# Kernel tuning notes

Hardware: AMD Instinct MI355X
Metric: run time of the kernel (lower is better)

Reference implementation:

```python
import jax, jax.numpy as jnp
import numpy as np

NUM_SLOTS = 8
SLOT_DIM = 64
HIDDEN_DIM = 128  # max(slot_dim, 128)
ITERS = 3
EPS = 1e-08
LN_EPS = 1e-05


def _ln(x, w, b):
    mu = jnp.mean(x, axis=-1, keepdims=True)
    var = jnp.mean(jnp.square(x - mu), axis=-1, keepdims=True)
    return (x - mu) * jax.lax.rsqrt(var + LN_EPS) * w + b


def setup_inputs() -> dict:
    key = jax.random.key(0)
    ks = jax.random.split(key, 16)
    b, n, d, h, n_s = 64, 4096, SLOT_DIM, HIDDEN_DIM, NUM_SLOTS
    s = 1.0 / np.sqrt(d)
    sh = 1.0 / np.sqrt(h)
    inp = {
        'inputs': jax.random.normal(ks[0], (b, n, d), jnp.float32),
        'mask': jax.random.randint(ks[1], (b, n), 0, 2, jnp.int32),
        'noise': jax.random.normal(ks[2], (b, n_s, d), jnp.float32),
        'slots_mu': jax.random.normal(ks[3], (1, 1, d), jnp.float32),
        'slots_sigma': jax.random.uniform(ks[4], (1, 1, d), jnp.float32),
        'Wq': jax.random.normal(ks[5], (d, d), jnp.float32) * s,
        'bq': jnp.zeros((d,), jnp.float32),
        'Wk': jax.random.normal(ks[6], (d, d), jnp.float32) * s,
        'bk': jnp.zeros((d,), jnp.float32),
        'Wv': jax.random.normal(ks[7], (d, d), jnp.float32) * s,
        'bv': jnp.zeros((d,), jnp.float32),
        'W_ih': jax.random.normal(ks[8], (3 * d, d), jnp.float32) * s,
        'b_ih': jnp.zeros((3 * d,), jnp.float32),
        'W_hh': jax.random.normal(ks[9], (3 * d, d), jnp.float32) * s,
        'b_hh': jnp.zeros((3 * d,), jnp.float32),
        'W1': jax.random.normal(ks[10], (h, d), jnp.float32) * s,
        'b1': jnp.zeros((h,), jnp.float32),
        'W2': jax.random.normal(ks[11], (d, h), jnp.float32) * sh,
        'b2': jnp.zeros((d,), jnp.float32),
        'ln_in_w': jnp.ones((d,), jnp.float32), 'ln_in_b': jnp.zeros((d,), jnp.float32),
        'ln_s_w': jnp.ones((d,), jnp.float32), 'ln_s_b': jnp.zeros((d,), jnp.float32),
        'ln_ff_w': jnp.ones((d,), jnp.float32), 'ln_ff_b': jnp.zeros((d,), jnp.float32),
    }
    return inp


def reference(inputs, mask, noise, slots_mu, slots_sigma, Wq, bq, Wk, bk, Wv, bv,
              W_ih, b_ih, W_hh, b_hh, W1, b1, W2, b2,
              ln_in_w, ln_in_b, ln_s_w, ln_s_b, ln_ff_w, ln_ff_b):
    b, n, d = inputs.shape
    scale = d ** (-0.5)
    # slots ~ Normal(mu, sigma) via reparameterization with fixed noise
    slots = slots_mu + slots_sigma * noise  # [b, n_s, d]
    m = (mask[:, :, None] != 0)  # [b, n, 1]
    x = _ln(inputs, ln_in_w, ln_in_b)
    k = x @ Wk.T + bk  # [b, n, d]
    v = x @ Wv.T + bv  # [b, n, d]
    for _ in range(ITERS):
        slots_prev = slots
        s_n = _ln(slots, ln_s_w, ln_s_b)
        q = s_n @ Wq.T + bq  # [b, n_s, d]
        dots = jnp.einsum('bid,bjd->bij', k, q) * scale  # [b, n, n_s]
        attn = jax.nn.softmax(dots, axis=-1) + EPS
        attn = jnp.where(m, attn, 0.0)
        attn = attn / jnp.sum(attn, axis=-2, keepdims=True)
        updates = jnp.einsum('bij,bid->bjd', attn, v)  # [b, n_s, d]
        # GRUCell(updates, slots_prev)
        gx = updates @ W_ih.T + b_ih  # [b, n_s, 3d]
        gh = slots_prev @ W_hh.T + b_hh
        xr, xz, xn = jnp.split(gx, 3, axis=-1)
        hr, hz, hn = jnp.split(gh, 3, axis=-1)
        r = jax.nn.sigmoid(xr + hr)
        z = jax.nn.sigmoid(xz + hz)
        nn_ = jnp.tanh(xn + r * hn)
        slots = (1.0 - z) * nn_ + z * slots_prev
        # residual MLP
        ff = _ln(slots, ln_ff_w, ln_ff_b)
        slots = slots + (jax.nn.relu(ff @ W1.T + b1) @ W2.T + b2)
    return slots
```

## Files before the change

kernel.cpp:

```cpp
#include <hip/hip_runtime.h>
#include <hip/hip_bf16.h>

typedef unsigned short u16;
typedef unsigned int u32;
typedef unsigned long long u64;

#define BB 64
#define NN 4096
#define DD 64
#define NSLOT 8
#define HH 128
#define NITER 3

#define BF16_ONES_PROBE 0x3F803F80u

#define OFF_BQ   53248
#define OFF_BK   53312
#define OFF_BV   53376
#define OFF_BIH  53440
#define OFF_BHH  53632
#define OFF_B1   53824
#define OFF_B2   53952
#define OFF_LIW  54016
#define OFF_LIB  54080
#define OFF_LSW  54144
#define OFF_LSB  54208
#define OFF_LFW  54272
#define OFF_LFB  54336
#define OFF_PK   58496

__device__ __forceinline__ float bf2f(u16 u) {
    union { u32 i; float f; } c; c.i = ((u32)u) << 16; return c.f;
}
__device__ __forceinline__ float bflo(u32 w) {
    union { u32 i; float f; } c; c.i = w << 16; return c.f;
}
__device__ __forceinline__ float bfhi(u32 w) {
    union { u32 i; float f; } c; c.i = w & 0xffff0000u; return c.f;
}
__device__ __forceinline__ u16 f2bf(float f) {
    __hip_bfloat16 h = __float2bfloat16(f);
    return *reinterpret_cast<u16*>(&h);
}
__device__ __forceinline__ float ldf(const void* p, int i, bool isbf) {
    return isbf ? bf2f(((const u16*)p)[i]) : ((const float*)p)[i];
}

__device__ __forceinline__ float wsum64(float x) {
    #pragma unroll
    for (int o = 32; o > 0; o >>= 1) x += __shfl_xor(x, o);
    return x;
}

__device__ __forceinline__ float ln64(float v, const float* __restrict__ g,
                                      const float* __restrict__ b, int lane) {
    float mu = wsum64(v) * (1.f / 64.f);
    float d = v - mu;
    float var = wsum64(d * d) * (1.f / 64.f);
    return d * rsqrtf(var + 1e-5f) * g[lane] + b[lane];
}

__device__ __forceinline__ float mat64q(const float* __restrict__ xs,
                                        const float* __restrict__ P,
                                        int lane, int wq) {
    const float4* p4 = (const float4*)P;
    const float4* x4 = (const float4*)xs;
    int c0 = wq << 2;
    float4 x0 = x4[c0], x1 = x4[c0 + 1], x2 = x4[c0 + 2], x3 = x4[c0 + 3];
    float4 w0 = p4[c0 * 64 + lane];
    float4 w1 = p4[(c0 + 1) * 64 + lane];
    float4 w2 = p4[(c0 + 2) * 64 + lane];
    float4 w3 = p4[(c0 + 3) * 64 + lane];
    float a0 = w0.x * x0.x + w0.y * x0.y + w0.z * x0.z + w0.w * x0.w;
    float a1 = w1.x * x1.x + w1.y * x1.y + w1.z * x1.z + w1.w * x1.w;
    float a2 = w2.x * x2.x + w2.y * x2.y + w2.z * x2.z + w2.w * x2.w;
    float a3 = w3.x * x3.x + w3.y * x3.y + w3.z * x3.z + w3.w * x3.w;
    return (a0 + a1) + (a2 + a3);
}

struct PrepArgs {
    const void* w[7];
    const void* v[13];
};

__global__ __launch_bounds__(256) void prep_w(PrepArgs a, float* __restrict__ wf,
                                              const u32* __restrict__ probe) {
    bool isbf = (*probe == BF16_ONES_PROBE);
    int idx = blockIdx.x * 256 + threadIdx.x;
    if (idx < 13 * 4096) {
        int blk = idx >> 12, r = idx & 4095;
        int c = r >> 8, rem = r & 255, j = rem >> 2, dd = rem & 3;
        int m = 4 * c + dd;
        float val;
        if      (blk == 0)  val = ldf(a.w[2], j * 64 + m, isbf);
        else if (blk == 1)  val = ldf(a.w[0], j * 64 + m, isbf);
        else if (blk == 2)  val = ldf(a.w[1], m * 64 + j, isbf);
        else if (blk < 6)   val = ldf(a.w[3], ((blk - 3) * 64 + j) * 64 + m, isbf);
        else if (blk < 9)   val = ldf(a.w[4], ((blk - 6) * 64 + j) * 64 + m, isbf);
        else if (blk < 11)  val = ldf(a.w[5], ((blk - 9) * 64 + j) * 64 + m, isbf);
        else                val = ldf(a.w[6], j * 128 + (blk - 11) * 64 + m, isbf);
        wf[OFF_PK + idx] = val;
    } else {
        int k = idx - 13 * 4096;
        const int voff[13] = {OFF_BQ, OFF_BK, OFF_BV, OFF_BIH, OFF_BHH, OFF_B1, OFF_B2,
                              OFF_LIW, OFF_LIB, OFF_LSW, OFF_LSB, OFF_LFW, OFF_LFB};
        const int vn[13]   = {64, 64, 64, 192, 192, 128, 64, 64, 64, 64, 64, 64, 64};
        #pragma unroll
        for (int t = 0; t < 13; t++) {
            if (k < vn[t]) { wf[voff[t] + k] = ldf(a.v[t], k, isbf); return; }
            k -= vn[t];
        }
    }
}

__device__ __forceinline__ void emit_qstate4(
        float qv, int b, int s, int bs, int lane, int wave,
        const float* __restrict__ wf, float* __restrict__ xa,
        float (*__restrict__ red)[64],
        float* __restrict__ gqp, float* __restrict__ Avec, float* __restrict__ Cvec) {
    if (wave == 0) xa[lane] = qv;
    __syncthreads();
    red[wave][lane] = mat64q(xa, wf + OFF_PK + 2 * 4096, lane, wave);
    __syncthreads();
    float qkv = red[0][lane] + red[1][lane] + red[2][lane] + red[3][lane];
    float gqv = wf[OFF_LIW + lane] * qkv;
    if (wave == 0) gqp[(b << 9) + (lane >> 2) * 32 + s * 4 + (lane & 3)] = gqv;
    float A  = wsum64(gqv);
    float bd = wsum64(qv * wf[OFF_BK + lane]);
    float cq = wsum64(wf[OFF_LIB + lane] * qkv);
    if (wave == 0 && lane == 0) { Avec[bs] = A; Cvec[bs] = cq + bd; }
}

__global__ __launch_bounds__(256, 1) void init_slots(
        const void* __restrict__ noise, const void* __restrict__ mu, const void* __restrict__ sg,
        const float* __restrict__ wf, float* __restrict__ slots,
        float* __restrict__ gqp, float* __restrict__ Avec, float* __restrict__ Cvec,
        float* __restrict__ acc1, float* __restrict__ ssv, float* __restrict__ A2v,
        const u32* __restrict__ probe) {
    __shared__ __align__(16) float xa[64];
    __shared__ float red[4][64];
    bool isbf = (*probe == BF16_ONES_PROBE);
    int bs = blockIdx.x;
    int b = bs >> 3, s = bs & 7;
    int tid = threadIdx.x, wave = tid >> 6, lane = tid & 63;
    int idx = bs * DD + lane;
    float sl = ldf(mu, lane, isbf) + ldf(sg, lane, isbf) * ldf(noise, idx, isbf);
    if (wave == 0) {
        slots[idx] = sl;
        acc1[idx] = 0.f;
        if (lane == 0) { ssv[bs] = 0.f; A2v[bs] = 0.f; }
    }
    float sn = ln64(sl, wf + OFF_LSW, wf + OFF_LSB, lane);
    if (wave == 0) xa[lane] = sn;
    __syncthreads();
    red[wave][lane] = mat64q(xa, wf + OFF_PK + 1 * 4096, lane, wave);
    __syncthreads();
    float qv = wf[OFF_BQ + lane] + red[0][lane] + red[1][lane] + red[2][lane] + red[3][lane];
    emit_qstate4(qv, b, s, bs, lane, wave, wf, xa, red, gqp, Avec, Cvec);
}

__global__ __launch_bounds__(256) void fused_attn(
        const void* __restrict__ xin, const int* __restrict__ mask,
        const float* __restrict__ gqp, const float* __restrict__ Avec,
        const float* __restrict__ Cvec,
        float* __restrict__ acc1, float* __restrict__ ssv, float* __restrict__ A2v,
        const u32* __restrict__ probe) {
    __shared__ float4 gq_s[128];
    __shared__ float4 aw4[256][2];
    __shared__ float racc[4][NSLOT][64];
    __shared__ float rss[4][NSLOT];
    __shared__ float rA2[4][NSLOT];
    __shared__ u64 wmask[4];

    bool isbf = (*probe == BF16_ONES_PROBE);
    int b = blockIdx.x >> 4;
    int base = (blockIdx.x & 15) << 8;
    int tid = threadIdx.x;
    int wave = tid >> 6, lane = tid & 63;

    if (tid < 128) gq_s[tid] = ((const float4*)(gqp + ((size_t)b << 9)))[tid];

    size_t gt = ((size_t)b << 12) + base + tid;
    int mk = mask[gt];
    uint4 xrg[8];
    if (mk && isbf) {
        const uint4* xr = (const uint4*)((const u16*)xin + gt * 64);
        #pragma unroll
        for (int i = 0; i < 8; i++) xrg[i] = xr[i];
    }
    __syncthreads();

    float sum = 0.f, sq = 0.f;
    float d[8] = {0.f, 0.f, 0.f, 0.f, 0.f, 0.f, 0.f, 0.f};
    if (mk) {
        if (isbf) {
            #pragma unroll
            for (int c = 0; c < 16; c++) {
                u32 wa = (c & 1) ? xrg[c >> 1].z : xrg[c >> 1].x;
                u32 wb = (c & 1) ? xrg[c >> 1].w : xrg[c >> 1].y;
                float x0 = bflo(wa), x1 = bfhi(wa), x2 = bflo(wb), x3 = bfhi(wb);
                sum += x0 + x1 + x2 + x3;
                sq  += x0 * x0 + x1 * x1 + x2 * x2 + x3 * x3;
                #pragma unroll
                for (int s = 0; s < 8; s++) {
                    float4 q = gq_s[c * 8 + s];
                    d[s] += q.x * x0 + q.y * x1 + q.z * x2 + q.w * x3;
                }
            }
        } else {
            const float4* xr = (const float4*)((const float*)xin + gt * 64);
            #pragma unroll
            for (int c = 0; c < 16; c++) {
                float4 xv = xr[c];
                sum += xv.x + xv.y + xv.z + xv.w;
                sq  += xv.x * xv.x + xv.y * xv.y + xv.z * xv.z + xv.w * xv.w;
                #pragma unroll
                for (int s = 0; s < 8; s++) {
                    float4 q = gq_s[c * 8 + s];
                    d[s] += q.x * xv.x + q.y * xv.y + q.z * xv.z + q.w * xv.w;
                }
            }
        }
    }
    float muv = sum * (1.f / 64.f);
    float var = sq * (1.f / 64.f) - muv * muv;
    float rs = rsqrtf(var + 1e-5f);
    const float* Av = Avec + (b << 3);
    const float* Cv = Cvec + (b << 3);
    #pragma unroll
    for (int s = 0; s < 8; s++)
        d[s] = 0.125f * (rs * d[s] - rs * muv * Av[s] + Cv[s]);

    float mx = d[0];
    #pragma unroll
    for (int s = 1; s < 8; s++) mx = fmaxf(mx, d[s]);
    float den = 0.f;
    #pragma unroll
    for (int s = 0; s < 8; s++) { d[s] = expf(d[s] - mx); den += d[s]; }
    float inv = 1.f / den;
    float attn[8], aw[8];
    #pragma unroll
    for (int s = 0; s < 8; s++) {
        attn[s] = (mk != 0) ? (d[s] * inv + 1e-8f) : 0.f;
        aw[s] = attn[s] * rs;
    }
    {
        float4 w0; w0.x = aw[0]; w0.y = aw[1]; w0.z = aw[2]; w0.w = aw[3];
        float4 w1; w1.x = aw[4]; w1.y = aw[5]; w1.z = aw[6]; w1.w = aw[7];
        aw4[tid][0] = w0;
        aw4[tid][1] = w1;
    }
    u64 bal = __ballot(mk != 0);
    if (lane == 0) wmask[wave] = bal;
    #pragma unroll
    for (int s = 0; s < 8; s++) {
        float t1 = wsum64(attn[s]);
        float t2 = wsum64(aw[s] * muv);
        if (lane == 0) { rss[wave][s] = t1; rA2[wave][s] = t2; }
    }
    __syncthreads();

    u64 bits = wmask[wave];
    float acc[8] = {0.f, 0.f, 0.f, 0.f, 0.f, 0.f, 0.f, 0.f};
    size_t rowbase = ((size_t)b << 12) + base + (wave << 6);
    const u16* xb16 = (const u16*)xin + rowbase * 64 + lane;
    const float* xf32 = (const float*)xin + rowbase * 64 + lane;
    #pragma unroll 8
    for (int t = 0; t < 64; t++) {
        if ((bits >> t) & 1ULL) {
            float xv = isbf ? bf2f(xb16[t * 64]) : xf32[t * 64];
            float4 a0 = aw4[(wave << 6) + t][0];
            float4 a1 = aw4[(wave << 6) + t][1];
            acc[0] += a0.x * xv; acc[1] += a0.y * xv;
            acc[2] += a0.z * xv; acc[3] += a0.w * xv;
            acc[4] += a1.x * xv; acc[5] += a1.y * xv;
            acc[6] += a1.z * xv; acc[7] += a1.w * xv;
        }
    }
    #pragma unroll
    for (int s = 0; s < 8; s++) racc[wave][s][lane] = acc[s];
    __syncthreads();
    if (wave == 0) {
        float* ag = acc1 + ((size_t)b << 9);
        #pragma unroll
        for (int s = 0; s < 8; s++) {
            float v = racc[0][s][lane] + racc[1][s][lane] + racc[2][s][lane] + racc[3][s][lane];
            atomicAdd(ag + s * 64 + lane, v);
        }
        if (lane < NSLOT) {
            float t1 = rss[0][lane] + rss[1][lane] + rss[2][lane] + rss[3][lane];
            float t2 = rA2[0][lane] + rA2[1][lane] + rA2[2][lane] + rA2[3][lane];
            atomicAdd(ssv + (b << 3) + lane, t1);
            atomicAdd(A2v + (b << 3) + lane, t2);
        }
    }
}

__global__ __launch_bounds__(256, 1) void finalize_k(
        const float* __restrict__ wf, float* __restrict__ acc1, float* __restrict__ ssv,
        float* __restrict__ A2v, float* __restrict__ slots,
        float* __restrict__ gqp, float* __restrict__ Avec, float* __restrict__ Cvec,
        void* __restrict__ out, int last, const u32* __restrict__ probe) {
    __shared__ __align__(16) float xa[64];
    __shared__ __align__(16) float xb[64];
    __shared__ float red[6][4][64];
    bool isbf = (*probe == BF16_ONES_PROBE);
    int bs = blockIdx.x;
    int b = bs >> 3, s = bs & 7;
    int tid = threadIdx.x, wave = tid >> 6, lane = tid & 63;
    int idx = bs * DD + lane;
    const float* P = wf + OFF_PK;

    float sm   = ssv[bs];
    float a2v_ = A2v[bs];
    float ac   = acc1[idx];
    float sp   = slots[idx];

    float un = wf[OFF_LIW + lane] * (ac - a2v_) / sm + wf[OFF_LIB + lane];
    if (wave == 0) xa[lane] = un;
    __syncthreads();
    if (wave == 0) {
        acc1[idx] = 0.f;
        if (lane == 0) { ssv[bs] = 0.f; A2v[bs] = 0.f; }
    }

    red[0][wave][lane] = mat64q(xa, P + 0 * 4096, lane, wave);
    __syncthreads();
    #define SUM4(k) (red[k][0][lane] + red[k][1][lane] + red[k][2][lane] + red[k][3][lane])
    float uv = wf[OFF_BV + lane] + SUM4(0);
    if (wave == 0) { xa[lane] = uv; xb[lane] = sp; }
    __syncthreads();

    red[0][wave][lane] = mat64q(xa, P + 3 * 4096, lane, wave);
    red[1][wave][lane] = mat64q(xa, P + 4 * 4096, lane, wave);
    red[2][wave][lane] = mat64q(xa, P + 5 * 4096, lane, wave);
    red[3][wave][lane] = mat64q(xb, P + 6 * 4096, lane, wave);
    red[4][wave][lane] = mat64q(xb, P + 7 * 4096, lane, wave);
    red[5][wave][lane] = mat64q(xb, P + 8 * 4096, lane, wave);
    __syncthreads();
    float gxr = wf[OFF_BIH + lane]       + SUM4(0);
    float gxz = wf[OFF_BIH + 64 + lane]  + SUM4(1);
    float gxn = wf[OFF_BIH + 128 + lane] + SUM4(2);
    float ghr = wf[OFF_BHH + lane]       + SUM4(3);
    float ghz = wf[OFF_BHH + 64 + lane]  + SUM4(4);
    float ghn = wf[OFF_BHH + 128 + lane] + SUM4(5);
    float r = 1.f / (1.f + expf(-(gxr + ghr)));
    float z = 1.f / (1.f + expf(-(gxz + ghz)));
    float nn = tanhf(gxn + r * ghn);
    float snew = (1.f - z) * nn + z * sp;

    float ff = ln64(snew, wf + OFF_LFW, wf + OFF_LFB, lane);
    if (wave == 0) xa[lane] = ff;
    __syncthreads();
    red[0][wave][lane] = mat64q(xa, P + 9 * 4096, lane, wave);
    red[1][wave][lane] = mat64q(xa, P + 10 * 4096, lane, wave);
    __syncthreads();
    float h1a = fmaxf(wf[OFF_B1 + lane] + SUM4(0), 0.f);
    float h1b = fmaxf(wf[OFF_B1 + 64 + lane] + SUM4(1), 0.f);
    if (wave == 0) { xa[lane] = h1a; xb[lane] = h1b; }
    __syncthreads();
    red[0][wave][lane] = mat64q(xa, P + 11 * 4096, lane, wave)
                       + mat64q(xb, P + 12 * 4096, lane, wave);
    __syncthreads();
    float o = snew + wf[OFF_B2 + lane] + SUM4(0);

    if (wave == 0) slots[idx] = o;
    if (last) {
        if (wave == 0) {
            if (isbf) ((u16*)out)[idx] = f2bf(o);
            else      ((float*)out)[idx] = o;
        }
    } else {
        float sn2 = ln64(o, wf + OFF_LSW, wf + OFF_LSB, lane);
        if (wave == 0) xa[lane] = sn2;
        __syncthreads();
        red[0][wave][lane] = mat64q(xa, P + 1 * 4096, lane, wave);
        __syncthreads();
        float qv = wf[OFF_BQ + lane] + SUM4(0);
        emit_qstate4(qv, b, s, bs, lane, wave, wf, xa, red[0], gqp, Avec, Cvec);
    }
    #undef SUM4
}

extern "C" void kernel_launch(void* const* d_in, const int* in_sizes, int n_in,
                              void* d_out, int out_size, void* d_ws, size_t ws_size,
                              hipStream_t stream) {
    const void* xin   = d_in[0];
    const int* mask   = (const int*)d_in[1];
    const void* noise = d_in[2];
    const void* mu    = d_in[3];
    const void* sg    = d_in[4];
    const u32* probe  = (const u32*)d_in[19];

    char* ws = (char*)d_ws;
    float* wf = (float*)ws;

    size_t o = 524288;
    float* gqp   = (float*)(ws + o); o += (size_t)BB * 512 * 4;
    float* Avec  = (float*)(ws + o); o += (size_t)BB * NSLOT * 4;
    float* Cvec  = (float*)(ws + o); o += (size_t)BB * NSLOT * 4;
    float* acc1  = (float*)(ws + o); o += (size_t)BB * NSLOT * DD * 4;
    float* ssv   = (float*)(ws + o); o += (size_t)BB * NSLOT * 4;
    float* A2v   = (float*)(ws + o); o += (size_t)BB * NSLOT * 4;
    float* slots = (float*)(ws + o); o += (size_t)BB * NSLOT * DD * 4;

    PrepArgs pa;
    pa.w[0] = d_in[5];
    pa.w[1] = d_in[7];
    pa.w[2] = d_in[9];
    pa.w[3] = d_in[11];
    pa.w[4] = d_in[13];
    pa.w[5] = d_in[15];
    pa.w[6] = d_in[17];
    static const int vidx[13] = {6, 8, 10, 12, 14, 16, 18, 19, 20, 21, 22, 23, 24};
    for (int j = 0; j < 13; j++) pa.v[j] = d_in[vidx[j]];

    prep_w<<<213, 256, 0, stream>>>(pa, wf, probe);
    init_slots<<<BB * NSLOT, 256, 0, stream>>>(noise, mu, sg, wf, slots,
                                               gqp, Avec, Cvec, acc1, ssv, A2v, probe);

    for (int it = 0; it < NITER; it++) {
        fused_attn<<<BB * 16, 256, 0, stream>>>(xin, mask, gqp, Avec, Cvec,
                                                acc1, ssv, A2v, probe);
        finalize_k<<<BB * NSLOT, 256, 0, stream>>>(wf, acc1, ssv, A2v, slots,
                                                   gqp, Avec, Cvec,
                                                   d_out, it == NITER - 1 ? 1 : 0, probe);
    }
}
```

Baseline: 260.1 us.

## Fuse slot finalize into attention kernel via last-block-done counter

Removes the separate finalize kernel per iteration. The last of the 16 attention blocks for each batch, detected through an atomic done-counter, now runs the GRU, MLP and next-query update in-kernel. Each wave handles two slots and does the small matvecs with wave shuffles instead of shared memory and block barriers. This saves three kernel launches and the tail waits between them. In exchange the finalize work is serialized into one block per batch, and correctness relies on atomic acquire/release ordering of the accumulator reads.

```diff
diff --git a/kernel.cpp b/kernel.cpp
--- a/kernel.cpp
+++ b/kernel.cpp
@@ -58,6 +58,18 @@
     float d = v - mu;
     float var = wsum64(d * d) * (1.f / 64.f);
     return d * rsqrtf(var + 1e-5f) * g[lane] + b[lane];
+}
+
+__device__ __forceinline__ float mat64p(float xv, const float* __restrict__ P, int lane) {
+    const float4* p4 = (const float4*)P;
+    float acc = 0.f;
+    #pragma unroll
+    for (int c = 0; c < 16; c++) {
+        float4 w = p4[c * 64 + lane];
+        acc += w.x * __shfl(xv, 4 * c + 0) + w.y * __shfl(xv, 4 * c + 1)
+             + w.z * __shfl(xv, 4 * c + 2) + w.w * __shfl(xv, 4 * c + 3);
+    }
+    return acc;
 }
 
 __device__ __forceinline__ float mat64q(const float* __restrict__ xs,
@@ -136,7 +148,7 @@
         const float* __restrict__ wf, float* __restrict__ slots,
         float* __restrict__ gqp, float* __restrict__ Avec, float* __restrict__ Cvec,
         float* __restrict__ acc1, float* __restrict__ ssv, float* __restrict__ A2v,
-        const u32* __restrict__ probe) {
+        u32* __restrict__ done_cnt, const u32* __restrict__ probe) {
     __shared__ __align__(16) float xa[64];
     __shared__ float red[4][64];
     bool isbf = (*probe == BF16_ONES_PROBE);
@@ -149,6 +161,7 @@
         slots[idx] = sl;
         acc1[idx] = 0.f;
         if (lane == 0) { ssv[bs] = 0.f; A2v[bs] = 0.f; }
+        if (s == 0 && lane < NITER) done_cnt[b * NITER + lane] = 0u;
     }
     float sn = ln64(sl, wf + OFF_LSW, wf + OFF_LSB, lane);
     if (wave == 0) xa[lane] = sn;
@@ -159,18 +172,115 @@
     emit_qstate4(qv, b, s, bs, lane, wave, wf, xa, red, gqp, Avec, Cvec);
 }
 
-__global__ __launch_bounds__(256) void fused_attn(
+__device__ void fin_slot(int b, int s, int lane, const float* __restrict__ wf,
+                         float* __restrict__ acc1, float* __restrict__ ssv,
+                         float* __restrict__ A2v, float* __restrict__ slots,
+                         float* __restrict__ gqp, float* __restrict__ Avec,
+                         float* __restrict__ Cvec, void* __restrict__ out,
+                         int last, bool isbf) {
+    int bs = b * NSLOT + s;
+    int idx = bs * DD + lane;
+    const float* P = wf + OFF_PK;
+
+    float sm = 0.f, a2 = 0.f;
+    if (lane == 0) {
+        sm = atomicExch(ssv + bs, 0.f);
+        a2 = atomicExch(A2v + bs, 0.f);
+    }
+    sm = __shfl(sm, 0);
+    a2 = __shfl(a2, 0);
+    float ac = atomicExch(acc1 + idx, 0.f);
+    float sp = slots[idx];
+
+    float un = wf[OFF_LIW + lane] * (ac - a2) / sm + wf[OFF_LIB + lane];
+    float uv = wf[OFF_BV + lane] + mat64p(un, P + 0 * 4096, lane);
+
+    float gxr = wf[OFF_BIH + lane], gxz = wf[OFF_BIH + 64 + lane], gxn = wf[OFF_BIH + 128 + lane];
+    float ghr = wf[OFF_BHH + lane], ghz = wf[OFF_BHH + 64 + lane], ghn = wf[OFF_BHH + 128 + lane];
+    const float4* pxr = (const float4*)(P + 3 * 4096);
+    const float4* pxz = (const float4*)(P + 4 * 4096);
+    const float4* pxn = (const float4*)(P + 5 * 4096);
+    const float4* phr = (const float4*)(P + 6 * 4096);
+    const float4* phz = (const float4*)(P + 7 * 4096);
+    const float4* phn = (const float4*)(P + 8 * 4096);
+    #pragma unroll
+    for (int c = 0; c < 16; c++) {
+        float u0 = __shfl(uv, 4 * c + 0), u1 = __shfl(uv, 4 * c + 1);
+        float u2 = __shfl(uv, 4 * c + 2), u3 = __shfl(uv, 4 * c + 3);
+        float p0 = __shfl(sp, 4 * c + 0), p1 = __shfl(sp, 4 * c + 1);
+        float p2 = __shfl(sp, 4 * c + 2), p3 = __shfl(sp, 4 * c + 3);
+        float4 a;
+        a = pxr[c * 64 + lane]; gxr += a.x * u0 + a.y * u1 + a.z * u2 + a.w * u3;
+        a = pxz[c * 64 + lane]; gxz += a.x * u0 + a.y * u1 + a.z * u2 + a.w * u3;
+        a = pxn[c * 64 + lane]; gxn += a.x * u0 + a.y * u1 + a.z * u2 + a.w * u3;
+        a = phr[c * 64 + lane]; ghr += a.x * p0 + a.y * p1 + a.z * p2 + a.w * p3;
+        a = phz[c * 64 + lane]; ghz += a.x * p0 + a.y * p1 + a.z * p2 + a.w * p3;
+        a = phn[c * 64 + lane]; ghn += a.x * p0 + a.y * p1 + a.z * p2 + a.w * p3;
+    }
+    float r = 1.f / (1.f + expf(-(gxr + ghr)));
+    float z = 1.f / (1.f + expf(-(gxz + ghz)));
+    float nn = tanhf(gxn + r * ghn);
+    float snew = (1.f - z) * nn + z * sp;
+
+    float ff = ln64(snew, wf + OFF_LFW, wf + OFF_LFB, lane);
+    float h1a = wf[OFF_B1 + lane], h1b = wf[OFF_B1 + 64 + lane];
+    const float4* p1a = (const float4*)(P + 9 * 4096);
+    const float4* p1b = (const float4*)(P + 10 * 4096);
+    #pragma unroll
+    for (int c = 0; c < 16; c++) {
+        float f0 = __shfl(ff, 4 * c + 0), f1 = __shfl(ff, 4 * c + 1);
+        float f2 = __shfl(ff, 4 * c + 2), f3 = __shfl(ff, 4 * c + 3);
+        float4 a;
+        a = p1a[c * 64 + lane]; h1a += a.x * f0 + a.y * f1 + a.z * f2 + a.w * f3;
+        a = p1b[c * 64 + lane]; h1b += a.x * f0 + a.y * f1 + a.z * f2 + a.w * f3;
+    }
+    h1a = fmaxf(h1a, 0.f);
+    h1b = fmaxf(h1b, 0.f);
+    float o = snew + wf[OFF_B2 + lane];
+    const float4* p2a = (const float4*)(P + 11 * 4096);
+    const float4* p2b = (const float4*)(P + 12 * 4096);
+    #pragma unroll
+    for (int c = 0; c < 16; c++) {
+        float a0 = __shfl(h1a, 4 * c + 0), a1 = __shfl(h1a, 4 * c + 1);
+        float a2_ = __shfl(h1a, 4 * c + 2), a3 = __shfl(h1a, 4 * c + 3);
+        float b0 = __shfl(h1b, 4 * c + 0), b1 = __shfl(h1b, 4 * c + 1);
+        float b2 = __shfl(h1b, 4 * c + 2), b3 = __shfl(h1b, 4 * c + 3);
+        float4 a;
+        a = p2a[c * 64 + lane]; o += a.x * a0 + a.y * a1 + a.z * a2_ + a.w * a3;
+        a = p2b[c * 64 + lane]; o += a.x * b0 + a.y * b1 + a.z * b2 + a.w * b3;
+    }
+
+    slots[idx] = o;
+    if (last) {
+        if (isbf) ((u16*)out)[idx] = f2bf(o);
+        else      ((float*)out)[idx] = o;
+    } else {
+        float sn2 = ln64(o, wf + OFF_LSW, wf + OFF_LSB, lane);
+        float qv = wf[OFF_BQ + lane] + mat64p(sn2, P + 1 * 4096, lane);
+        float qkv = mat64p(qv, P + 2 * 4096, lane);
+        float gqv = wf[OFF_LIW + lane] * qkv;
+        gqp[(b << 9) + (lane >> 2) * 32 + s * 4 + (lane & 3)] = gqv;
+        float A  = wsum64(gqv);
+        float bd = wsum64(qv * wf[OFF_BK + lane]);
+        float cq = wsum64(wf[OFF_LIB + lane] * qkv);
+        if (lane == 0) { Avec[bs] = A; Cvec[bs] = cq + bd; }
+    }
+}
+
+__global__ __launch_bounds__(256) void attn_fin(
         const void* __restrict__ xin, const int* __restrict__ mask,
-        const float* __restrict__ gqp, const float* __restrict__ Avec,
-        const float* __restrict__ Cvec,
+        const float* __restrict__ wf,
+        float* __restrict__ gqp, float* __restrict__ Avec, float* __restrict__ Cvec,
         float* __restrict__ acc1, float* __restrict__ ssv, float* __restrict__ A2v,
-        const u32* __restrict__ probe) {
+        float* __restrict__ slots, void* __restrict__ out,
+        u32* __restrict__ done_cnt, const u32* __restrict__ probe, int it) {
     __shared__ float4 gq_s[128];
     __shared__ float4 aw4[256][2];
     __shared__ float racc[4][NSLOT][64];
     __shared__ float rss[4][NSLOT];
     __shared__ float rA2[4][NSLOT];
     __shared__ u64 wmask[4];
+    __shared__ int do_fin;
 
     bool isbf = (*probe == BF16_ONES_PROBE);
     int b = blockIdx.x >> 4;
@@ -294,92 +404,20 @@
             atomicAdd(A2v + (b << 3) + lane, t2);
         }
     }
-}
-
-__global__ __launch_bounds__(256, 1) void finalize_k(
-        const float* __restrict__ wf, float* __restrict__ acc1, float* __restrict__ ssv,
-        float* __restrict__ A2v, float* __restrict__ slots,
-        float* __restrict__ gqp, float* __restrict__ Avec, float* __restrict__ Cvec,
-        void* __restrict__ out, int last, const u32* __restrict__ probe) {
-    __shared__ __align__(16) float xa[64];
-    __shared__ __align__(16) float xb[64];
-    __shared__ float red[6][4][64];
-    bool isbf = (*probe == BF16_ONES_PROBE);
-    int bs = blockIdx.x;
-    int b = bs >> 3, s = bs & 7;
-    int tid = threadIdx.x, wave = tid >> 6, lane = tid & 63;
-    int idx = bs * DD + lane;
-    const float* P = wf + OFF_PK;
-
-    float sm   = ssv[bs];
-    float a2v_ = A2v[bs];
-    float ac   = acc1[idx];
-    float sp   = slots[idx];
-
-    float un = wf[OFF_LIW + lane] * (ac - a2v_) / sm + wf[OFF_LIB + lane];
-    if (wave == 0) xa[lane] = un;
-    __syncthreads();
-    if (wave == 0) {
-        acc1[idx] = 0.f;
-        if (lane == 0) { ssv[bs] = 0.f; A2v[bs] = 0.f; }
-    }
-
-    red[0][wave][lane] = mat64q(xa, P + 0 * 4096, lane, wave);
-    __syncthreads();
-    #define SUM4(k) (red[k][0][lane] + red[k][1][lane] + red[k][2][lane] + red[k][3][lane])
-    float uv = wf[OFF_BV + lane] + SUM4(0);
-    if (wave == 0) { xa[lane] = uv; xb[lane] = sp; }
-    __syncthreads();
-
-    red[0][wave][lane] = mat64q(xa, P + 3 * 4096, lane, wave);
-    red[1][wave][lane] = mat64q(xa, P + 4 * 4096, lane, wave);
-    red[2][wave][lane] = mat64q(xa, P + 5 * 4096, lane, wave);
-    red[3][wave][lane] = mat64q(xb, P + 6 * 4096, lane, wave);
-    red[4][wave][lane] = mat64q(xb, P + 7 * 4096, lane, wave);
-    red[5][wave][lane] = mat64q(xb, P + 8 * 4096, lane, wave);
-    __syncthreads();
-    float gxr = wf[OFF_BIH + lane]       + SUM4(0);
-    float gxz = wf[OFF_BIH + 64 + lane]  + SUM4(1);
-    float gxn = wf[OFF_BIH + 128 + lane] + SUM4(2);
-    float ghr = wf[OFF_BHH + lane]       + SUM4(3);
-    float ghz = wf[OFF_BHH + 64 + lane]  + SUM4(4);
-    float ghn = wf[OFF_BHH + 128 + lane] + SUM4(5);
-    float r = 1.f / (1.f + expf(-(gxr + ghr)));
-    float z = 1.f / (1.f + expf(-(gxz + ghz)));
-    float nn = tanhf(gxn + r * ghn);
-    float snew = (1.f - z) * nn + z * sp;
-
-    float ff = ln64(snew, wf + OFF_LFW, wf + OFF_LFB, lane);
-    if (wave == 0) xa[lane] = ff;
-    __syncthreads();
-    red[0][wave][lane] = mat64q(xa, P + 9 * 4096, lane, wave);
-    red[1][wave][lane] = mat64q(xa, P + 10 * 4096, lane, wave);
-    __syncthreads();
-    float h1a = fmaxf(wf[OFF_B1 + lane] + SUM4(0), 0.f);
-    float h1b = fmaxf(wf[OFF_B1 + 64 + lane] + SUM4(1), 0.f);
-    if (wave == 0) { xa[lane] = h1a; xb[lane] = h1b; }
-    __syncthreads();
-    red[0][wave][lane] = mat64q(xa, P + 11 * 4096, lane, wave)
-                       + mat64q(xb, P + 12 * 4096, lane, wave);
-    __syncthreads();
-    float o = snew + wf[OFF_B2 + lane] + SUM4(0);
-
-    if (wave == 0) slots[idx] = o;
-    if (last) {
-        if (wave == 0) {
-            if (isbf) ((u16*)out)[idx] = f2bf(o);
-            else      ((float*)out)[idx] = o;
-        }
-    } else {
-        float sn2 = ln64(o, wf + OFF_LSW, wf + OFF_LSB, lane);
-        if (wave == 0) xa[lane] = sn2;
-        __syncthreads();
-        red[0][wave][lane] = mat64q(xa, P + 1 * 4096, lane, wave);
-        __syncthreads();
-        float qv = wf[OFF_BQ + lane] + SUM4(0);
-        emit_qstate4(qv, b, s, bs, lane, wave, wf, xa, red[0], gqp, Avec, Cvec);
-    }
-    #undef SUM4
+
+    if (tid == 0) {
+        u32 old = __hip_atomic_fetch_add(done_cnt + b * NITER + it, 1u,
+                                         __ATOMIC_ACQ_REL, __HIP_MEMORY_SCOPE_AGENT);
+        do_fin = (old == 15u) ? 1 : 0;
+    }
+    __syncthreads();
+    if (do_fin) {
+        int last = (it == NITER - 1) ? 1 : 0;
+        fin_slot(b, (wave << 1),     lane, wf, acc1, ssv, A2v, slots,
+                 gqp, Avec, Cvec, out, last, isbf);
+        fin_slot(b, (wave << 1) + 1, lane, wf, acc1, ssv, A2v, slots,
+                 gqp, Avec, Cvec, out, last, isbf);
+    }
 }
 
 extern "C" void kernel_launch(void* const* d_in, const int* in_sizes, int n_in,
@@ -403,6 +441,7 @@
     float* ssv   = (float*)(ws + o); o += (size_t)BB * NSLOT * 4;
     float* A2v   = (float*)(ws + o); o += (size_t)BB * NSLOT * 4;
     float* slots = (float*)(ws + o); o += (size_t)BB * NSLOT * DD * 4;
+    u32* done_cnt = (u32*)(ws + o);  o += 1024;
 
     PrepArgs pa;
     pa.w[0] = d_in[5];
@@ -417,13 +456,12 @@
 
     prep_w<<<213, 256, 0, stream>>>(pa, wf, probe);
     init_slots<<<BB * NSLOT, 256, 0, stream>>>(noise, mu, sg, wf, slots,
-                                               gqp, Avec, Cvec, acc1, ssv, A2v, probe);
+                                               gqp, Avec, Cvec, acc1, ssv, A2v,
+                                               done_cnt, probe);
 
     for (int it = 0; it < NITER; it++) {
-        fused_attn<<<BB * 16, 256, 0, stream>>>(xin, mask, gqp, Avec, Cvec,
-                                                acc1, ssv, A2v, probe);
-        finalize_k<<<BB * NSLOT, 256, 0, stream>>>(wf, acc1, ssv, A2v, slots,
-                                                   gqp, Avec, Cvec,
-                                                   d_out, it == NITER - 1 ? 1 : 0, probe);
-    }
-}
+        attn_fin<<<BB * 16, 256, 0, stream>>>(xin, mask, wf, gqp, Avec, Cvec,
+                                              acc1, ssv, A2v, slots, d_out,
+                                              done_cnt, probe, it);
+    }
+}
```

After: 606.9 us. 133% more time.
